# Kernel tuning notes

Hardware: AMD Instinct MI355X
Metric: run time of the kernel (lower is better)

The kernel has to match this reference:

```python
import jax, jax.numpy as jnp
import numpy as np

B, C, L, H, W, O = 1024, 256, 128, 256, 3, 256  # batch cols, channels, levels, hidden, window, output
N_LAYERS = 3


def setup_inputs() -> dict:
    key = jax.random.key(0)
    ks = jax.random.split(key, 12)
    in0 = C * W          # layer-0 input features after sliding window
    inr = 2 * H          # input features for layers > 0 (bi-dir concat)
    def wscale(fan_in):
        return 1.0 / np.sqrt(fan_in)
    inputs = jax.random.normal(ks[0], (B, C, L), dtype=jnp.float32)
    w_fw0 = jax.random.normal(ks[1], (in0 + H, 4 * H), jnp.float32) * wscale(in0 + H)
    b_fw0 = jnp.zeros((4 * H,), jnp.float32)
    w_bw0 = jax.random.normal(ks[2], (in0 + H, 4 * H), jnp.float32) * wscale(in0 + H)
    b_bw0 = jnp.zeros((4 * H,), jnp.float32)
    w_fw_rest = jax.random.normal(ks[3], (N_LAYERS - 1, inr + H, 4 * H), jnp.float32) * wscale(inr + H)
    b_fw_rest = jnp.zeros((N_LAYERS - 1, 4 * H), jnp.float32)
    w_bw_rest = jax.random.normal(ks[4], (N_LAYERS - 1, inr + H, 4 * H), jnp.float32) * wscale(inr + H)
    b_bw_rest = jnp.zeros((N_LAYERS - 1, 4 * H), jnp.float32)
    w_out = jax.random.normal(ks[5], (2 * H, O), jnp.float32) * wscale(2 * H)
    b_out = jnp.zeros((O,), jnp.float32)
    return dict(inputs=inputs, w_fw0=w_fw0, b_fw0=b_fw0, w_bw0=w_bw0, b_bw0=b_bw0,
                w_fw_rest=w_fw_rest, b_fw_rest=b_fw_rest, w_bw_rest=w_bw_rest,
                b_bw_rest=b_bw_rest, w_out=w_out, b_out=b_out)


def _lstm(xs, w, b, reverse):
    # xs: [L, B, F] time-major. haiku hk.LSTM gate order i, g, f, o with +1 forget bias.
    h0 = jnp.zeros((xs.shape[1], H), xs.dtype)
    def step(carry, x):
        h, c = carry
        gated = jnp.concatenate([x, h], axis=-1) @ w + b
        i, g, f, o = jnp.split(gated, 4, axis=-1)
        c = jax.nn.sigmoid(f + 1.0) * c + jax.nn.sigmoid(i) * jnp.tanh(g)
        h = jax.nn.sigmoid(o) * jnp.tanh(c)
        return (h, c), h
    _, ys = jax.lax.scan(step, (h0, h0), xs, reverse=reverse)
    return ys  # [L, B, H], aligned with input positions (matches hk.dynamic_unroll reverse)


def reference(inputs, w_fw0, b_fw0, w_bw0, b_bw0, w_fw_rest, b_fw_rest,
              w_bw_rest, b_bw_rest, w_out, b_out):
    x = jnp.swapaxes(inputs, 1, 2)  # [B, L, C] (original transposes [C, L] -> [L, C])
    # sliding_window_reshape over the level axis
    pad_start = (W - 1) // 2
    pad_end = W - 1 - pad_start
    xp = jnp.pad(x, ((0, 0), (pad_start, pad_end), (0, 0)))
    idx = jnp.arange(W)[None, :] + jnp.arange(L)[:, None]  # [L, W]
    xw = xp[:, idx, :]                                     # [B, L, W, C]
    xw = xw.reshape(x.shape[0], L, W * C)                  # row-major (window, channel) flatten
    xs = jnp.swapaxes(xw, 0, 1)                            # [L, B, W*C] time-major

    fw = _lstm(xs, w_fw0, b_fw0, reverse=False)
    bw = _lstm(xs, w_bw0, b_bw0, reverse=True)
    xs = jnp.concatenate([fw, bw], axis=-1)                # [L, B, 2H]
    for k in range(N_LAYERS - 1):
        fw = _lstm(xs, w_fw_rest[k], b_fw_rest[k], reverse=False)
        bw = _lstm(xs, w_bw_rest[k], b_bw_rest[k], reverse=True)
        xs = jnp.concatenate([fw, bw], axis=-1)

    out = xs @ w_out + b_out                               # [L, B, O]
    return jnp.transpose(out, (1, 2, 0))                   # [B, O, L] (original returns [O, L])
```

## Files before the change

kernel.cpp:

```cpp
#include <hip/hip_runtime.h>
#include <cstdint>

#define DEVI __device__ __forceinline__

typedef __bf16 bf16x8 __attribute__((ext_vector_type(8)));
typedef float f32x4 __attribute__((ext_vector_type(4)));

DEVI unsigned short f2b(float f) {
    unsigned int u = __builtin_bit_cast(unsigned int, f);
    unsigned int r = (u + 0x7FFFu + ((u >> 16) & 1u)) >> 16;
    return (unsigned short)r;
}
DEVI float b2f(unsigned short h) {
    unsigned int u = ((unsigned int)h) << 16;
    return __builtin_bit_cast(float, u);
}
DEVI float sigm(float x) { return 1.0f / (1.0f + __expf(-x)); }
DEVI float tanh_f(float x) {
    float e = __expf(-2.0f * fabsf(x));
    float r = (1.0f - e) / (1.0f + e);
    return x < 0.0f ? -r : r;
}

DEVI void gload_lds16(const unsigned short* g, unsigned short* l) {
    typedef __attribute__((address_space(1))) void gv_t;
    typedef __attribute__((address_space(3))) void lv_t;
    gv_t* gp = (gv_t*)(uintptr_t)g;
    lv_t* lp = (lv_t*)(unsigned int)(uintptr_t)l;
    __builtin_amdgcn_global_load_lds(gp, lp, 16, 0, 0);
}

__global__ void k_tin(const float* __restrict__ in, unsigned short* __restrict__ xT) {
    __shared__ float tile[32][33];
    int c0 = blockIdx.x * 32, t0 = blockIdx.y * 32, b = blockIdx.z;
    int tx = threadIdx.x, ty = threadIdx.y;
#pragma unroll
    for (int i = 0; i < 4; ++i) {
        int c = c0 + ty + i * 8;
        int t = t0 + tx;
        float v = 0.0f;
        if (t >= 1 && t <= 128) v = in[((size_t)b * 256 + c) * 128 + (t - 1)];
        tile[ty + i * 8][tx] = v;
    }
    __syncthreads();
#pragma unroll
    for (int i = 0; i < 4; ++i) {
        int t = t0 + ty + i * 8;
        int c = c0 + tx;
        if (t < 130) xT[((size_t)t * 1024 + b) * 256 + c] = f2b(tile[tx][ty + i * 8]);
    }
}

__global__ void k_wt(const float* __restrict__ w, unsigned short* __restrict__ wt, int K, int N) {
    __shared__ float tile[32][33];
    int n0 = blockIdx.x * 32, k0 = blockIdx.y * 32;
    int tx = threadIdx.x, ty = threadIdx.y;
#pragma unroll
    for (int i = 0; i < 4; ++i)
        tile[ty + i * 8][tx] = w[(size_t)(k0 + ty + i * 8) * N + n0 + tx];
    __syncthreads();
#pragma unroll
    for (int i = 0; i < 4; ++i)
        wt[(size_t)(n0 + ty + i * 8) * K + k0 + tx] = f2b(tile[tx][ty + i * 8]);
}

#define BM 128
#define BN 128
#define BKg 64

template <int MODE, int F32OUT, int BIAS>
__global__ __launch_bounds__(256) void kgemm(const unsigned short* __restrict__ A,
                                             const unsigned short* __restrict__ Wt,
                                             void* __restrict__ Cout,
                                             const float* __restrict__ bias,
                                             int Mtiles, int Ntiles, int KT, int strideA,
                                             int strideB, int N, int tbase) {
    __shared__ unsigned short As[BM * BKg];
    __shared__ unsigned short Bs[BN * BKg];

    int nwg = Mtiles * Ntiles;
    int q = nwg >> 3;
    int orig = blockIdx.x;
    int wg = (orig & 7) * q + (orig >> 3);
    int tn = wg % Ntiles, tm = wg / Ntiles;

    int tid = threadIdx.x;
    int wid = tid >> 6, lane = tid & 63;
    int srow = lane >> 3, skb = lane & 7;
    int lh = lane & 15, lq = lane >> 4;

    f32x4 acc[4][4] = {};
    int m0 = tm * BM;
    int t0 = m0 >> 10, b0 = m0 & 1023;
    int wr = wid >> 1, wc = wid & 1;

    for (int k0 = 0; k0 < KT; k0 += BKg) {
        const unsigned short* Abase;
        int rs;
        if (MODE == 1) {
            int w = k0 >> 8, c0 = k0 & 255;
            Abase = A + ((size_t)((tbase + t0 + w) * 1024 + b0)) * 256 + c0;
            rs = 256;
        } else {
            Abase = A + (size_t)m0 * strideA + k0;
            rs = strideA;
        }
        const unsigned short* Bbase = Wt + (size_t)(tn * BN) * strideB + k0;
#pragma unroll
        for (int c = 0; c < 4; ++c) {
            int chunk = c * 4 + wid;
            int row = chunk * 8 + srow;
            int kbs = skb ^ (row & 7);
            gload_lds16(Abase + (size_t)row * rs + kbs * 8, &As[chunk * 512]);
        }
#pragma unroll
        for (int c = 0; c < 4; ++c) {
            int chunk = c * 4 + wid;
            int row = chunk * 8 + srow;
            int kbs = skb ^ (row & 7);
            gload_lds16(Bbase + (size_t)row * strideB + kbs * 8, &Bs[chunk * 512]);
        }
        __syncthreads();
#pragma unroll
        for (int kk = 0; kk < 2; ++kk) {
            bf16x8 af[4], bfv[4];
            int kc = kk * 4 + lq;
#pragma unroll
            for (int i = 0; i < 4; ++i) {
                int m = wr * 64 + i * 16 + lh;
                af[i] = *(const bf16x8*)((const char*)As + m * 128 + ((kc ^ (m & 7)) * 16));
            }
#pragma unroll
            for (int j = 0; j < 4; ++j) {
                int n = wc * 64 + j * 16 + lh;
                bfv[j] = *(const bf16x8*)((const char*)Bs + n * 128 + ((kc ^ (n & 7)) * 16));
            }
#pragma unroll
            for (int i = 0; i < 4; ++i)
#pragma unroll
                for (int j = 0; j < 4; ++j)
                    acc[i][j] = __builtin_amdgcn_mfma_f32_16x16x32_bf16(af[i], bfv[j], acc[i][j], 0, 0, 0);
        }
        __syncthreads();
    }
#pragma unroll
    for (int i = 0; i < 4; ++i) {
#pragma unroll
        for (int j = 0; j < 4; ++j) {
            int colg = tn * BN + wc * 64 + j * 16 + lh;
            float bv = BIAS ? bias[colg] : 0.0f;
#pragma unroll
            for (int r = 0; r < 4; ++r) {
                int rowg = m0 + wr * 64 + i * 16 + lq * 4 + r;
                float v = acc[i][j][r] + bv;
                if (F32OUT)
                    ((float*)Cout)[(size_t)rowg * N + colg] = v;
                else
                    ((unsigned short*)Cout)[(size_t)rowg * N + colg] = f2b(v);
            }
        }
    }
}

__global__ __launch_bounds__(512) void klstm(const unsigned short* __restrict__ gxf,
                                             const unsigned short* __restrict__ gxb,
                                             const unsigned short* __restrict__ wtf,
                                             const unsigned short* __restrict__ wtb,
                                             const float* __restrict__ bf_,
                                             const float* __restrict__ bb_,
                                             unsigned short* __restrict__ xs_out,
                                             unsigned short* __restrict__ hst,
                                             float* __restrict__ cst,
                                             int I, int KS, int s0, int Tc) {
    __shared__ unsigned short h_lds[32 * 256];
    int dir = blockIdx.y;
    int b0 = blockIdx.x * 32;
    const unsigned short* gx = dir ? gxb : gxf;
    const unsigned short* wt = dir ? wtb : wtf;
    const float* bias = dir ? bb_ : bf_;
    const unsigned short* wh = wt + I;

    int tid = threadIdx.x, wid = tid >> 6, lane = tid & 63;
    int lh = lane & 15, lq = lane >> 4;

    float c_reg[2][2][4] = {};
    if (s0 == 0) {
        for (int i = tid; i < 32 * 256; i += 512) h_lds[i] = 0;
    } else {
        for (int i = tid; i < 32 * 256; i += 512) {
            int row = i >> 8, col = i & 255;
            *(unsigned short*)((char*)h_lds + row * 512 + (((col >> 3) ^ (row & 7)) * 16) +
                               (col & 7) * 2) = hst[((size_t)dir * 1024 + b0 + row) * 256 + col];
        }
#pragma unroll
        for (int mf = 0; mf < 2; ++mf)
#pragma unroll
            for (int r = 0; r < 4; ++r)
#pragma unroll
                for (int p = 0; p < 2; ++p) {
                    int row = mf * 16 + lq * 4 + r;
                    int col = wid * 32 + p * 16 + lh;
                    c_reg[mf][p][r] = cst[((size_t)dir * 1024 + b0 + row) * 256 + col];
                }
    }
    float bia[2], big[2], bif[2], bio[2];
#pragma unroll
    for (int p = 0; p < 2; ++p) {
        int col = wid * 32 + p * 16 + lh;
        bia[p] = bias[col];
        big[p] = bias[256 + col];
        bif[p] = bias[512 + col];
        bio[p] = bias[768 + col];
    }
    __syncthreads();

    for (int s = s0; s < s0 + Tc; ++s) {
        int t = dir ? (127 - s) : s;
        int gloc = dir ? (s0 + Tc - 1 - s) : (s - s0);

        bf16x8 afr[2][8];
#pragma unroll
        for (int mf = 0; mf < 2; ++mf)
#pragma unroll
            for (int kf = 0; kf < 8; ++kf) {
                int m = mf * 16 + lh;
                int kc = kf * 4 + lq;
                afr[mf][kf] = *(const bf16x8*)((const char*)h_lds + m * 512 + ((kc ^ (m & 7)) * 16));
            }
        __syncthreads();

        f32x4 acc[2][8] = {};
#pragma unroll
        for (int kf = 0; kf < 8; ++kf) {
#pragma unroll
            for (int nf = 0; nf < 8; ++nf) {
                int g = nf >> 1, p = nf & 1;
                int n = g * 256 + wid * 32 + p * 16 + lh;
                bf16x8 bfr = *(const bf16x8*)(wh + (size_t)n * KS + kf * 32 + lq * 8);
                acc[0][nf] = __builtin_amdgcn_mfma_f32_16x16x32_bf16(afr[0][kf], bfr, acc[0][nf], 0, 0, 0);
                acc[1][nf] = __builtin_amdgcn_mfma_f32_16x16x32_bf16(afr[1][kf], bfr, acc[1][nf], 0, 0, 0);
            }
        }

#pragma unroll
        for (int mf = 0; mf < 2; ++mf) {
#pragma unroll
            for (int r = 0; r < 4; ++r) {
                int row = mf * 16 + lq * 4 + r;
                size_t gxrow = ((size_t)gloc * 1024 + b0 + row) * 1024;
#pragma unroll
                for (int p = 0; p < 2; ++p) {
                    int col = wid * 32 + p * 16 + lh;
                    float gi = acc[mf][0 + p][r] + b2f(gx[gxrow + col]) + bia[p];
                    float gg = acc[mf][2 + p][r] + b2f(gx[gxrow + 256 + col]) + big[p];
                    float gf = acc[mf][4 + p][r] + b2f(gx[gxrow + 512 + col]) + bif[p];
                    float go = acc[mf][6 + p][r] + b2f(gx[gxrow + 768 + col]) + bio[p];
                    float cv = sigm(gf + 1.0f) * c_reg[mf][p][r] + sigm(gi) * tanh_f(gg);
                    c_reg[mf][p][r] = cv;
                    float hv = sigm(go) * tanh_f(cv);
                    unsigned short hb = f2b(hv);
                    *(unsigned short*)((char*)h_lds + row * 512 + (((col >> 3) ^ (row & 7)) * 16) +
                                       (col & 7) * 2) = hb;
                    xs_out[((size_t)t * 1024 + b0 + row) * 512 + dir * 256 + col] = hb;
                }
            }
        }
        __syncthreads();
    }

    for (int i = tid; i < 32 * 256; i += 512) {
        int row = i >> 8, col = i & 255;
        hst[((size_t)dir * 1024 + b0 + row) * 256 + col] =
            *(const unsigned short*)((const char*)h_lds + row * 512 +
                                     (((col >> 3) ^ (row & 7)) * 16) + (col & 7) * 2);
    }
#pragma unroll
    for (int mf = 0; mf < 2; ++mf)
#pragma unroll
        for (int r = 0; r < 4; ++r)
#pragma unroll
            for (int p = 0; p < 2; ++p) {
                int row = mf * 16 + lq * 4 + r;
                int col = wid * 32 + p * 16 + lh;
                cst[((size_t)dir * 1024 + b0 + row) * 256 + col] = c_reg[mf][p][r];
            }
}

__global__ void k_tout(const float* __restrict__ tmp, float* __restrict__ out) {
    __shared__ float tile[32][33];
    int o0 = blockIdx.x * 32, l0 = blockIdx.y * 32, b = blockIdx.z;
    int tx = threadIdx.x, ty = threadIdx.y;
#pragma unroll
    for (int i = 0; i < 4; ++i)
        tile[ty + i * 8][tx] = tmp[((size_t)(l0 + ty + i * 8) * 1024 + b) * 256 + o0 + tx];
    __syncthreads();
#pragma unroll
    for (int i = 0; i < 4; ++i)
        out[((size_t)b * 256 + o0 + ty + i * 8) * 128 + l0 + tx] = tile[tx][ty + i * 8];
}

extern "C" void kernel_launch(void* const* d_in, const int* in_sizes, int n_in,
                              void* d_out, int out_size, void* d_ws, size_t ws_size,
                              hipStream_t stream) {
    const float* inp  = (const float*)d_in[0];
    const float* wfw0 = (const float*)d_in[1];
    const float* bfw0 = (const float*)d_in[2];
    const float* wbw0 = (const float*)d_in[3];
    const float* bbw0 = (const float*)d_in[4];
    const float* wfwr = (const float*)d_in[5];
    const float* bfwr = (const float*)d_in[6];
    const float* wbwr = (const float*)d_in[7];
    const float* bbwr = (const float*)d_in[8];
    const float* wout = (const float*)d_in[9];
    const float* bout = (const float*)d_in[10];

    char* ws = (char*)d_ws;
    size_t o = 0;
    auto alloc = [&](size_t bytes) {
        void* p = ws + o;
        o += (bytes + 255) & ~(size_t)255;
        return p;
    };
    unsigned short* wt0f = (unsigned short*)alloc((size_t)1024 * 1024 * 2);
    unsigned short* wt0b = (unsigned short*)alloc((size_t)1024 * 1024 * 2);
    unsigned short* wt1f = (unsigned short*)alloc((size_t)1024 * 768 * 2);
    unsigned short* wt1b = (unsigned short*)alloc((size_t)1024 * 768 * 2);
    unsigned short* wt2f = (unsigned short*)alloc((size_t)1024 * 768 * 2);
    unsigned short* wt2b = (unsigned short*)alloc((size_t)1024 * 768 * 2);
    unsigned short* wto  = (unsigned short*)alloc((size_t)256 * 512 * 2);
    unsigned short* hst  = (unsigned short*)alloc((size_t)2 * 1024 * 256 * 2);
    float*          cst  = (float*)alloc((size_t)2 * 1024 * 256 * 4);
    unsigned short* xsa  = (unsigned short*)alloc((size_t)131072 * 512 * 2);
    unsigned short* xsb  = (unsigned short*)alloc((size_t)131072 * 512 * 2);
    unsigned short* xT   = xsb;
    float*          otmp = (float*)xsb;

    size_t base = o;
    int Tc = 128;
    while (Tc > 1 && base + (size_t)Tc * 4 * 1024 * 1024 > ws_size) Tc >>= 1;
    unsigned short* gxf = (unsigned short*)alloc((size_t)Tc * 1024 * 1024 * 2);
    unsigned short* gxb = (unsigned short*)alloc((size_t)Tc * 1024 * 1024 * 2);

    dim3 tb(32, 8);
    k_tin<<<dim3(8, 5, 1024), tb, 0, stream>>>(inp, xT);
    k_wt<<<dim3(32, 32), tb, 0, stream>>>(wfw0, wt0f, 1024, 1024);
    k_wt<<<dim3(32, 32), tb, 0, stream>>>(wbw0, wt0b, 1024, 1024);
    k_wt<<<dim3(32, 24), tb, 0, stream>>>(wfwr, wt1f, 768, 1024);
    k_wt<<<dim3(32, 24), tb, 0, stream>>>(wbwr, wt1b, 768, 1024);
    k_wt<<<dim3(32, 24), tb, 0, stream>>>(wfwr + (size_t)768 * 1024, wt2f, 768, 1024);
    k_wt<<<dim3(32, 24), tb, 0, stream>>>(wbwr + (size_t)768 * 1024, wt2b, 768, 1024);
    k_wt<<<dim3(8, 16), tb, 0, stream>>>(wout, wto, 512, 256);

    int Mt = Tc * 8, grid = Tc * 64;
    for (int s0 = 0; s0 < 128; s0 += Tc) {
        int tbw = 128 - s0 - Tc;
        kgemm<1, 0, 0><<<grid, 256, 0, stream>>>(xT, wt0f, gxf, nullptr, Mt, 8, 768, 256, 1024, 1024, s0);
        kgemm<1, 0, 0><<<grid, 256, 0, stream>>>(xT, wt0b, gxb, nullptr, Mt, 8, 768, 256, 1024, 1024, tbw);
        klstm<<<dim3(32, 2), 512, 0, stream>>>(gxf, gxb, wt0f, wt0b, bfw0, bbw0, xsa, hst, cst, 768, 1024, s0, Tc);
    }
    for (int s0 = 0; s0 < 128; s0 += Tc) {
        int tbw = 128 - s0 - Tc;
        kgemm<0, 0, 0><<<grid, 256, 0, stream>>>(xsa + (size_t)s0 * 1024 * 512, wt1f, gxf, nullptr, Mt, 8, 512, 512, 768, 1024, 0);
        kgemm<0, 0, 0><<<grid, 256, 0, stream>>>(xsa + (size_t)tbw * 1024 * 512, wt1b, gxb, nullptr, Mt, 8, 512, 512, 768, 1024, 0);
        klstm<<<dim3(32, 2), 512, 0, stream>>>(gxf, gxb, wt1f, wt1b, bfwr, bbwr, xsb, hst, cst, 512, 768, s0, Tc);
    }
    for (int s0 = 0; s0 < 128; s0 += Tc) {
        int tbw = 128 - s0 - Tc;
        kgemm<0, 0, 0><<<grid, 256, 0, stream>>>(xsb + (size_t)s0 * 1024 * 512, wt2f, gxf, nullptr, Mt, 8, 512, 512, 768, 1024, 0);
        kgemm<0, 0, 0><<<grid, 256, 0, stream>>>(xsb + (size_t)tbw * 1024 * 512, wt2b, gxb, nullptr, Mt, 8, 512, 512, 768, 1024, 0);
        klstm<<<dim3(32, 2), 512, 0, stream>>>(gxf, gxb, wt2f, wt2b, bfwr + 1024, bbwr + 1024, xsa, hst, cst, 512, 768, s0, Tc);
    }
    kgemm<0, 1, 1><<<2048, 256, 0, stream>>>(xsa, wto, otmp, bout, 1024, 2, 512, 512, 512, 256, 0);
    k_tout<<<dim3(8, 4, 1024), tb, 0, stream>>>(otmp, (float*)d_out);
}
```

Baseline: 9.077 ms.

## Fuse input projection into persistent bidirectional LSTM kernel with double-buffered x staging

Drops the separate per-chunk input-projection GEMMs, the gx buffers and the h/c state save/restore. A single 64-block kernel per layer now runs all 128 steps, multiplying the concatenated [x, h] by the full weight each step. The next timestep's input is prefetched into LDS with async global-to-LDS loads while the current step computes. This removes the gate-preactivation round trip through memory and many launches. In exchange, the non-recurrent GEMM work is serialized onto only 64 workgroups, and far more weight bytes are read from cache per step. Sigmoid and tanh divisions are also swapped for hardware reciprocal.

```diff
diff --git a/kernel.cpp b/kernel.cpp
--- a/kernel.cpp
+++ b/kernel.cpp
@@ -11,14 +11,11 @@
     unsigned int r = (u + 0x7FFFu + ((u >> 16) & 1u)) >> 16;
     return (unsigned short)r;
 }
-DEVI float b2f(unsigned short h) {
-    unsigned int u = ((unsigned int)h) << 16;
-    return __builtin_bit_cast(float, u);
-}
-DEVI float sigm(float x) { return 1.0f / (1.0f + __expf(-x)); }
+DEVI float frcp(float x) { return __builtin_amdgcn_rcpf(x); }
+DEVI float sigm(float x) { return frcp(1.0f + __expf(-x)); }
 DEVI float tanh_f(float x) {
     float e = __expf(-2.0f * fabsf(x));
-    float r = (1.0f - e) / (1.0f + e);
+    float r = (1.0f - e) * frcp(1.0f + e);
     return x < 0.0f ? -r : r;
 }
 
@@ -162,47 +159,55 @@
     }
 }
 
-__global__ __launch_bounds__(512) void klstm(const unsigned short* __restrict__ gxf,
-                                             const unsigned short* __restrict__ gxb,
-                                             const unsigned short* __restrict__ wtf,
-                                             const unsigned short* __restrict__ wtb,
-                                             const float* __restrict__ bf_,
-                                             const float* __restrict__ bb_,
-                                             unsigned short* __restrict__ xs_out,
-                                             unsigned short* __restrict__ hst,
-                                             float* __restrict__ cst,
-                                             int I, int KS, int s0, int Tc) {
+template <int KX, int WIN>
+DEVI void stage_x(const unsigned short* __restrict__ xin, int t, int b0,
+                  unsigned short* xbuf, int tid) {
+    constexpr int CH = KX / 16;
+    int wid = tid >> 6, lane = tid & 63;
+#pragma unroll
+    for (int c = wid; c < CH; c += 8) {
+        int e = c * 512 + lane * 8;
+        int row = e / KX;
+        int slot = (e - row * KX) >> 3;
+        int ss = (slot & ~7) | ((slot & 7) ^ (row & 7));
+        int col = ss << 3;
+        const unsigned short* src;
+        if (WIN) {
+            int w = col >> 8, cc = col & 255;
+            src = xin + ((size_t)((t + w) * 1024 + b0 + row)) * 256 + cc;
+        } else {
+            src = xin + ((size_t)t * 1024 + b0 + row) * (size_t)KX + col;
+        }
+        gload_lds16(src, xbuf + c * 512);
+    }
+}
+
+template <int KX, int WIN>
+__global__ __launch_bounds__(512) void klstm_f(const unsigned short* __restrict__ xin,
+                                               const unsigned short* __restrict__ wtf,
+                                               const unsigned short* __restrict__ wtb,
+                                               const float* __restrict__ bf_,
+                                               const float* __restrict__ bb_,
+                                               unsigned short* __restrict__ xs_out) {
+    constexpr int KS = KX + 256;
+    constexpr int KF_X = KX / 32;
     __shared__ unsigned short h_lds[32 * 256];
-    int dir = blockIdx.y;
-    int b0 = blockIdx.x * 32;
-    const unsigned short* gx = dir ? gxb : gxf;
+    __shared__ unsigned short xb[2][32 * KX];
+
+    int bid = blockIdx.x;
+    int xcd = bid & 7;
+    int dir = xcd >> 2;
+    int idx = (bid >> 3) * 4 + (xcd & 3);
+    int b0 = idx * 32;
     const unsigned short* wt = dir ? wtb : wtf;
     const float* bias = dir ? bb_ : bf_;
-    const unsigned short* wh = wt + I;
 
     int tid = threadIdx.x, wid = tid >> 6, lane = tid & 63;
     int lh = lane & 15, lq = lane >> 4;
 
+    for (int i = tid; i < 32 * 256; i += 512) h_lds[i] = 0;
+
     float c_reg[2][2][4] = {};
-    if (s0 == 0) {
-        for (int i = tid; i < 32 * 256; i += 512) h_lds[i] = 0;
-    } else {
-        for (int i = tid; i < 32 * 256; i += 512) {
-            int row = i >> 8, col = i & 255;
-            *(unsigned short*)((char*)h_lds + row * 512 + (((col >> 3) ^ (row & 7)) * 16) +
-                               (col & 7) * 2) = hst[((size_t)dir * 1024 + b0 + row) * 256 + col];
-        }
-#pragma unroll
-        for (int mf = 0; mf < 2; ++mf)
-#pragma unroll
-            for (int r = 0; r < 4; ++r)
-#pragma unroll
-                for (int p = 0; p < 2; ++p) {
-                    int row = mf * 16 + lq * 4 + r;
-                    int col = wid * 32 + p * 16 + lh;
-                    c_reg[mf][p][r] = cst[((size_t)dir * 1024 + b0 + row) * 256 + col];
-                }
-    }
     float bia[2], big[2], bif[2], bio[2];
 #pragma unroll
     for (int p = 0; p < 2; ++p) {
@@ -212,49 +217,75 @@
         bif[p] = bias[512 + col];
         bio[p] = bias[768 + col];
     }
+    stage_x<KX, WIN>(xin, dir ? 127 : 0, b0, &xb[0][0], tid);
     __syncthreads();
 
-    for (int s = s0; s < s0 + Tc; ++s) {
+    for (int s = 0; s < 128; ++s) {
         int t = dir ? (127 - s) : s;
-        int gloc = dir ? (s0 + Tc - 1 - s) : (s - s0);
-
-        bf16x8 afr[2][8];
-#pragma unroll
-        for (int mf = 0; mf < 2; ++mf)
-#pragma unroll
-            for (int kf = 0; kf < 8; ++kf) {
-                int m = mf * 16 + lh;
-                int kc = kf * 4 + lq;
-                afr[mf][kf] = *(const bf16x8*)((const char*)h_lds + m * 512 + ((kc ^ (m & 7)) * 16));
-            }
-        __syncthreads();
+        int tnx = dir ? (t > 0 ? t - 1 : 0) : (t < 127 ? t + 1 : 127);
+        const unsigned short* xcur = &xb[s & 1][0];
+
+        stage_x<KX, WIN>(xin, tnx, b0, &xb[(s & 1) ^ 1][0], tid);
 
         f32x4 acc[2][8] = {};
-#pragma unroll
-        for (int kf = 0; kf < 8; ++kf) {
+#pragma unroll 4
+        for (int kf = 0; kf < KF_X; ++kf) {
+            int kc = kf * 4 + lq;
+            bf16x8 a0, a1;
+            {
+                int m = lh;
+                int ss = (kc & ~7) | ((kc & 7) ^ (m & 7));
+                a0 = *(const bf16x8*)((const char*)xcur + m * (KX * 2) + ss * 16);
+            }
+            {
+                int m = 16 + lh;
+                int ss = (kc & ~7) | ((kc & 7) ^ (m & 7));
+                a1 = *(const bf16x8*)((const char*)xcur + m * (KX * 2) + ss * 16);
+            }
 #pragma unroll
             for (int nf = 0; nf < 8; ++nf) {
                 int g = nf >> 1, p = nf & 1;
                 int n = g * 256 + wid * 32 + p * 16 + lh;
-                bf16x8 bfr = *(const bf16x8*)(wh + (size_t)n * KS + kf * 32 + lq * 8);
-                acc[0][nf] = __builtin_amdgcn_mfma_f32_16x16x32_bf16(afr[0][kf], bfr, acc[0][nf], 0, 0, 0);
-                acc[1][nf] = __builtin_amdgcn_mfma_f32_16x16x32_bf16(afr[1][kf], bfr, acc[1][nf], 0, 0, 0);
-            }
-        }
+                bf16x8 bfr = *(const bf16x8*)(wt + (size_t)n * KS + kf * 32 + lq * 8);
+                acc[0][nf] = __builtin_amdgcn_mfma_f32_16x16x32_bf16(a0, bfr, acc[0][nf], 0, 0, 0);
+                acc[1][nf] = __builtin_amdgcn_mfma_f32_16x16x32_bf16(a1, bfr, acc[1][nf], 0, 0, 0);
+            }
+        }
+#pragma unroll
+        for (int kf = 0; kf < 8; ++kf) {
+            int kc = kf * 4 + lq;
+            bf16x8 a0, a1;
+            {
+                int m = lh;
+                a0 = *(const bf16x8*)((const char*)h_lds + m * 512 + ((kc ^ (m & 7)) * 16));
+            }
+            {
+                int m = 16 + lh;
+                a1 = *(const bf16x8*)((const char*)h_lds + m * 512 + ((kc ^ (m & 7)) * 16));
+            }
+#pragma unroll
+            for (int nf = 0; nf < 8; ++nf) {
+                int g = nf >> 1, p = nf & 1;
+                int n = g * 256 + wid * 32 + p * 16 + lh;
+                bf16x8 bfr = *(const bf16x8*)(wt + (size_t)n * KS + KX + kf * 32 + lq * 8);
+                acc[0][nf] = __builtin_amdgcn_mfma_f32_16x16x32_bf16(a0, bfr, acc[0][nf], 0, 0, 0);
+                acc[1][nf] = __builtin_amdgcn_mfma_f32_16x16x32_bf16(a1, bfr, acc[1][nf], 0, 0, 0);
+            }
+        }
+        __syncthreads();
 
 #pragma unroll
         for (int mf = 0; mf < 2; ++mf) {
 #pragma unroll
             for (int r = 0; r < 4; ++r) {
                 int row = mf * 16 + lq * 4 + r;
-                size_t gxrow = ((size_t)gloc * 1024 + b0 + row) * 1024;
 #pragma unroll
                 for (int p = 0; p < 2; ++p) {
                     int col = wid * 32 + p * 16 + lh;
-                    float gi = acc[mf][0 + p][r] + b2f(gx[gxrow + col]) + bia[p];
-                    float gg = acc[mf][2 + p][r] + b2f(gx[gxrow + 256 + col]) + big[p];
-                    float gf = acc[mf][4 + p][r] + b2f(gx[gxrow + 512 + col]) + bif[p];
-                    float go = acc[mf][6 + p][r] + b2f(gx[gxrow + 768 + col]) + bio[p];
+                    float gi = acc[mf][0 + p][r] + bia[p];
+                    float gg = acc[mf][2 + p][r] + big[p];
+                    float gf = acc[mf][4 + p][r] + bif[p];
+                    float go = acc[mf][6 + p][r] + bio[p];
                     float cv = sigm(gf + 1.0f) * c_reg[mf][p][r] + sigm(gi) * tanh_f(gg);
                     c_reg[mf][p][r] = cv;
                     float hv = sigm(go) * tanh_f(cv);
@@ -267,23 +298,6 @@
         }
         __syncthreads();
     }
-
-    for (int i = tid; i < 32 * 256; i += 512) {
-        int row = i >> 8, col = i & 255;
-        hst[((size_t)dir * 1024 + b0 + row) * 256 + col] =
-            *(const unsigned short*)((const char*)h_lds + row * 512 +
-                                     (((col >> 3) ^ (row & 7)) * 16) + (col & 7) * 2);
-    }
-#pragma unroll
-    for (int mf = 0; mf < 2; ++mf)
-#pragma unroll
-        for (int r = 0; r < 4; ++r)
-#pragma unroll
-            for (int p = 0; p < 2; ++p) {
-                int row = mf * 16 + lq * 4 + r;
-                int col = wid * 32 + p * 16 + lh;
-                cst[((size_t)dir * 1024 + b0 + row) * 256 + col] = c_reg[mf][p][r];
-            }
 }
 
 __global__ void k_tout(const float* __restrict__ tmp, float* __restrict__ out) {
@@ -328,18 +342,10 @@
     unsigned short* wt2f = (unsigned short*)alloc((size_t)1024 * 768 * 2);
     unsigned short* wt2b = (unsigned short*)alloc((size_t)1024 * 768 * 2);
     unsigned short* wto  = (unsigned short*)alloc((size_t)256 * 512 * 2);
-    unsigned short* hst  = (unsigned short*)alloc((size_t)2 * 1024 * 256 * 2);
-    float*          cst  = (float*)alloc((size_t)2 * 1024 * 256 * 4);
     unsigned short* xsa  = (unsigned short*)alloc((size_t)131072 * 512 * 2);
-    unsigned short* xsb  = (unsigned short*)alloc((size_t)131072 * 512 * 2);
-    unsigned short* xT   = xsb;
-    float*          otmp = (float*)xsb;
-
-    size_t base = o;
-    int Tc = 128;
-    while (Tc > 1 && base + (size_t)Tc * 4 * 1024 * 1024 > ws_size) Tc >>= 1;
-    unsigned short* gxf = (unsigned short*)alloc((size_t)Tc * 1024 * 1024 * 2);
-    unsigned short* gxb = (unsigned short*)alloc((size_t)Tc * 1024 * 1024 * 2);
+    unsigned short* xsbR = (unsigned short*)alloc((size_t)131072 * 512 * 2);
+    unsigned short* xT   = xsbR;
+    float*          otmp = (float*)xsbR;
 
     dim3 tb(32, 8);
     k_tin<<<dim3(8, 5, 1024), tb, 0, stream>>>(inp, xT);
@@ -351,25 +357,10 @@
     k_wt<<<dim3(32, 24), tb, 0, stream>>>(wbwr + (size_t)768 * 1024, wt2b, 768, 1024);
     k_wt<<<dim3(8, 16), tb, 0, stream>>>(wout, wto, 512, 256);
 
-    int Mt = Tc * 8, grid = Tc * 64;
-    for (int s0 = 0; s0 < 128; s0 += Tc) {
-        int tbw = 128 - s0 - Tc;
-        kgemm<1, 0, 0><<<grid, 256, 0, stream>>>(xT, wt0f, gxf, nullptr, Mt, 8, 768, 256, 1024, 1024, s0);
-        kgemm<1, 0, 0><<<grid, 256, 0, stream>>>(xT, wt0b, gxb, nullptr, Mt, 8, 768, 256, 1024, 1024, tbw);
-        klstm<<<dim3(32, 2), 512, 0, stream>>>(gxf, gxb, wt0f, wt0b, bfw0, bbw0, xsa, hst, cst, 768, 1024, s0, Tc);
-    }
-    for (int s0 = 0; s0 < 128; s0 += Tc) {
-        int tbw = 128 - s0 - Tc;
-        kgemm<0, 0, 0><<<grid, 256, 0, stream>>>(xsa + (size_t)s0 * 1024 * 512, wt1f, gxf, nullptr, Mt, 8, 512, 512, 768, 1024, 0);
-        kgemm<0, 0, 0><<<grid, 256, 0, stream>>>(xsa + (size_t)tbw * 1024 * 512, wt1b, gxb, nullptr, Mt, 8, 512, 512, 768, 1024, 0);
-        klstm<<<dim3(32, 2), 512, 0, stream>>>(gxf, gxb, wt1f, wt1b, bfwr, bbwr, xsb, hst, cst, 512, 768, s0, Tc);
-    }
-    for (int s0 = 0; s0 < 128; s0 += Tc) {
-        int tbw = 128 - s0 - Tc;
-        kgemm<0, 0, 0><<<grid, 256, 0, stream>>>(xsb + (size_t)s0 * 1024 * 512, wt2f, gxf, nullptr, Mt, 8, 512, 512, 768, 1024, 0);
-        kgemm<0, 0, 0><<<grid, 256, 0, stream>>>(xsb + (size_t)tbw * 1024 * 512, wt2b, gxb, nullptr, Mt, 8, 512, 512, 768, 1024, 0);
-        klstm<<<dim3(32, 2), 512, 0, stream>>>(gxf, gxb, wt2f, wt2b, bfwr + 1024, bbwr + 1024, xsa, hst, cst, 512, 768, s0, Tc);
-    }
+    klstm_f<768, 1><<<64, 512, 0, stream>>>(xT, wt0f, wt0b, bfw0, bbw0, xsa);
+    klstm_f<512, 0><<<64, 512, 0, stream>>>(xsa, wt1f, wt1b, bfwr, bbwr, xsbR);
+    klstm_f<512, 0><<<64, 512, 0, stream>>>(xsbR, wt2f, wt2b, bfwr + 1024, bbwr + 1024, xsa);
+
     kgemm<0, 1, 1><<<2048, 256, 0, stream>>>(xsa, wto, otmp, bout, 1024, 2, 512, 512, 512, 256, 0);
     k_tout<<<dim3(8, 4, 1024), tb, 0, stream>>>(otmp, (float*)d_out);
 }
```

After: 22.69 ms. +149.9%, slower.

## Split LSTM weights, fuse fw/bw input GEMMs, software-pipeline recurrent MFMA loads

Applied to the files above, without the earlier changes.

Splits each layer's weights into separate input and recurrent blocks, with forward and backward stacked. When the workspace allows, one GEMM per layer computes both directions' input projections into an interleaved 2048-wide buffer. The recurrent kernel now streams recurrent weights through a three-slot register ring and H fragments through a double buffer, overlapping global and LDS loads with MFMAs, and it prefetches the gate inputs before the activations. Sigmoid and tanh use a hardware reciprocal instead of division, which adds register pressure and slightly lowers accuracy.

```diff
diff --git a/kernel.cpp b/kernel.cpp
--- a/kernel.cpp
+++ b/kernel.cpp
@@ -15,10 +15,11 @@
     unsigned int u = ((unsigned int)h) << 16;
     return __builtin_bit_cast(float, u);
 }
-DEVI float sigm(float x) { return 1.0f / (1.0f + __expf(-x)); }
+DEVI float frcp(float x) { return __builtin_amdgcn_rcpf(x); }
+DEVI float sigm(float x) { return frcp(1.0f + __expf(-x)); }
 DEVI float tanh_f(float x) {
     float e = __expf(-2.0f * fabsf(x));
-    float r = (1.0f - e) / (1.0f + e);
+    float r = (1.0f - e) * frcp(1.0f + e);
     return x < 0.0f ? -r : r;
 }
 
@@ -162,23 +163,20 @@
     }
 }
 
-__global__ __launch_bounds__(512) void klstm(const unsigned short* __restrict__ gxf,
-                                             const unsigned short* __restrict__ gxb,
-                                             const unsigned short* __restrict__ wtf,
-                                             const unsigned short* __restrict__ wtb,
-                                             const float* __restrict__ bf_,
-                                             const float* __restrict__ bb_,
-                                             unsigned short* __restrict__ xs_out,
-                                             unsigned short* __restrict__ hst,
-                                             float* __restrict__ cst,
-                                             int I, int KS, int s0, int Tc) {
+__global__ __launch_bounds__(512, 2) void klstm_p(const unsigned short* __restrict__ gxf,
+                                                  const unsigned short* __restrict__ gxb, int GS,
+                                                  const unsigned short* __restrict__ wth,
+                                                  const float* __restrict__ bf_,
+                                                  const float* __restrict__ bb_,
+                                                  unsigned short* __restrict__ xs_out,
+                                                  unsigned short* __restrict__ hst,
+                                                  float* __restrict__ cst, int s0, int Tc) {
     __shared__ unsigned short h_lds[32 * 256];
     int dir = blockIdx.y;
     int b0 = blockIdx.x * 32;
     const unsigned short* gx = dir ? gxb : gxf;
-    const unsigned short* wt = dir ? wtb : wtf;
+    const unsigned short* wh = wth + (size_t)dir * 1024 * 256;
     const float* bias = dir ? bb_ : bf_;
-    const unsigned short* wh = wt + I;
 
     int tid = threadIdx.x, wid = tid >> 6, lane = tid & 63;
     int lh = lane & 15, lq = lane >> 4;
@@ -212,49 +210,82 @@
         bif[p] = bias[512 + col];
         bio[p] = bias[768 + col];
     }
+    const unsigned short* wb[8];
+#pragma unroll
+    for (int nf = 0; nf < 8; ++nf) {
+        int g = nf >> 1, p = nf & 1;
+        int n = g * 256 + wid * 32 + p * 16 + lh;
+        wb[nf] = wh + (size_t)n * 256 + lq * 8;
+    }
     __syncthreads();
 
     for (int s = s0; s < s0 + Tc; ++s) {
         int t = dir ? (127 - s) : s;
         int gloc = dir ? (s0 + Tc - 1 - s) : (s - s0);
 
-        bf16x8 afr[2][8];
+        f32x4 acc[2][8] = {};
+        bf16x8 wreg[3][8];
+        bf16x8 afr[2][2];
+
+#define LDW(KF, SLOT)                                                       \
+    {                                                                       \
+        _Pragma("unroll") for (int nf = 0; nf < 8; ++nf) wreg[SLOT][nf] =   \
+            *(const bf16x8*)(wb[nf] + (KF)*32);                             \
+    }
+#define LDA(KF, SLOT)                                                        \
+    {                                                                        \
+        int kc = (KF)*4 + lq;                                                \
+        _Pragma("unroll") for (int mf = 0; mf < 2; ++mf) {                   \
+            int m = mf * 16 + lh;                                            \
+            afr[SLOT][mf] = *(const bf16x8*)((const char*)h_lds + m * 512 +  \
+                                             ((kc ^ (m & 7)) * 16));         \
+        }                                                                    \
+    }
+        LDW(0, 0);
+        LDW(1, 1);
+        LDA(0, 0);
+#pragma unroll
+        for (int kf = 0; kf < 8; ++kf) {
+            if (kf < 6) LDW(kf + 2, (kf + 2) % 3);
+            if (kf < 7) LDA(kf + 1, (kf + 1) & 1);
+#pragma unroll
+            for (int nf = 0; nf < 8; ++nf) {
+                acc[0][nf] = __builtin_amdgcn_mfma_f32_16x16x32_bf16(afr[kf & 1][0], wreg[kf % 3][nf],
+                                                                    acc[0][nf], 0, 0, 0);
+                acc[1][nf] = __builtin_amdgcn_mfma_f32_16x16x32_bf16(afr[kf & 1][1], wreg[kf % 3][nf],
+                                                                    acc[1][nf], 0, 0, 0);
+            }
+        }
+#undef LDW
+#undef LDA
+        __syncthreads();
+
+        unsigned short gu[2][2][4][4];
 #pragma unroll
         for (int mf = 0; mf < 2; ++mf)
-#pragma unroll
-            for (int kf = 0; kf < 8; ++kf) {
-                int m = mf * 16 + lh;
-                int kc = kf * 4 + lq;
-                afr[mf][kf] = *(const bf16x8*)((const char*)h_lds + m * 512 + ((kc ^ (m & 7)) * 16));
-            }
-        __syncthreads();
-
-        f32x4 acc[2][8] = {};
-#pragma unroll
-        for (int kf = 0; kf < 8; ++kf) {
-#pragma unroll
-            for (int nf = 0; nf < 8; ++nf) {
-                int g = nf >> 1, p = nf & 1;
-                int n = g * 256 + wid * 32 + p * 16 + lh;
-                bf16x8 bfr = *(const bf16x8*)(wh + (size_t)n * KS + kf * 32 + lq * 8);
-                acc[0][nf] = __builtin_amdgcn_mfma_f32_16x16x32_bf16(afr[0][kf], bfr, acc[0][nf], 0, 0, 0);
-                acc[1][nf] = __builtin_amdgcn_mfma_f32_16x16x32_bf16(afr[1][kf], bfr, acc[1][nf], 0, 0, 0);
-            }
-        }
-
-#pragma unroll
-        for (int mf = 0; mf < 2; ++mf) {
 #pragma unroll
             for (int r = 0; r < 4; ++r) {
                 int row = mf * 16 + lq * 4 + r;
-                size_t gxrow = ((size_t)gloc * 1024 + b0 + row) * 1024;
+                const unsigned short* gp = gx + ((size_t)gloc * 1024 + b0 + row) * GS;
 #pragma unroll
                 for (int p = 0; p < 2; ++p) {
                     int col = wid * 32 + p * 16 + lh;
-                    float gi = acc[mf][0 + p][r] + b2f(gx[gxrow + col]) + bia[p];
-                    float gg = acc[mf][2 + p][r] + b2f(gx[gxrow + 256 + col]) + big[p];
-                    float gf = acc[mf][4 + p][r] + b2f(gx[gxrow + 512 + col]) + bif[p];
-                    float go = acc[mf][6 + p][r] + b2f(gx[gxrow + 768 + col]) + bio[p];
+#pragma unroll
+                    for (int g = 0; g < 4; ++g) gu[mf][p][r][g] = gp[g * 256 + col];
+                }
+            }
+#pragma unroll
+        for (int mf = 0; mf < 2; ++mf) {
+#pragma unroll
+            for (int r = 0; r < 4; ++r) {
+                int row = mf * 16 + lq * 4 + r;
+#pragma unroll
+                for (int p = 0; p < 2; ++p) {
+                    int col = wid * 32 + p * 16 + lh;
+                    float gi = acc[mf][0 + p][r] + b2f(gu[mf][p][r][0]) + bia[p];
+                    float gg = acc[mf][2 + p][r] + b2f(gu[mf][p][r][1]) + big[p];
+                    float gf = acc[mf][4 + p][r] + b2f(gu[mf][p][r][2]) + bif[p];
+                    float go = acc[mf][6 + p][r] + b2f(gu[mf][p][r][3]) + bio[p];
                     float cv = sigm(gf + 1.0f) * c_reg[mf][p][r] + sigm(gi) * tanh_f(gg);
                     c_reg[mf][p][r] = cv;
                     float hv = sigm(go) * tanh_f(cv);
@@ -321,55 +352,73 @@
         o += (bytes + 255) & ~(size_t)255;
         return p;
     };
-    unsigned short* wt0f = (unsigned short*)alloc((size_t)1024 * 1024 * 2);
-    unsigned short* wt0b = (unsigned short*)alloc((size_t)1024 * 1024 * 2);
-    unsigned short* wt1f = (unsigned short*)alloc((size_t)1024 * 768 * 2);
-    unsigned short* wt1b = (unsigned short*)alloc((size_t)1024 * 768 * 2);
-    unsigned short* wt2f = (unsigned short*)alloc((size_t)1024 * 768 * 2);
-    unsigned short* wt2b = (unsigned short*)alloc((size_t)1024 * 768 * 2);
+    unsigned short* wtx0 = (unsigned short*)alloc((size_t)2048 * 768 * 2);
+    unsigned short* wtx1 = (unsigned short*)alloc((size_t)2048 * 512 * 2);
+    unsigned short* wtx2 = (unsigned short*)alloc((size_t)2048 * 512 * 2);
+    unsigned short* wth0 = (unsigned short*)alloc((size_t)2048 * 256 * 2);
+    unsigned short* wth1 = (unsigned short*)alloc((size_t)2048 * 256 * 2);
+    unsigned short* wth2 = (unsigned short*)alloc((size_t)2048 * 256 * 2);
     unsigned short* wto  = (unsigned short*)alloc((size_t)256 * 512 * 2);
     unsigned short* hst  = (unsigned short*)alloc((size_t)2 * 1024 * 256 * 2);
     float*          cst  = (float*)alloc((size_t)2 * 1024 * 256 * 4);
     unsigned short* xsa  = (unsigned short*)alloc((size_t)131072 * 512 * 2);
-    unsigned short* xsb  = (unsigned short*)alloc((size_t)131072 * 512 * 2);
-    unsigned short* xT   = xsb;
-    float*          otmp = (float*)xsb;
+    unsigned short* xsbR = (unsigned short*)alloc((size_t)131072 * 512 * 2);
+    unsigned short* xT   = xsbR;
+    float*          otmp = (float*)xsbR;
 
     size_t base = o;
     int Tc = 128;
-    while (Tc > 1 && base + (size_t)Tc * 4 * 1024 * 1024 > ws_size) Tc >>= 1;
-    unsigned short* gxf = (unsigned short*)alloc((size_t)Tc * 1024 * 1024 * 2);
-    unsigned short* gxb = (unsigned short*)alloc((size_t)Tc * 1024 * 1024 * 2);
+    while (Tc > 1 && base + (size_t)Tc * 1024 * 2048 * 2 > ws_size) Tc >>= 1;
+    bool fused = (Tc == 128);
+    unsigned short* gx  = (unsigned short*)alloc((size_t)Tc * 1024 * 2048 * 2);
+    unsigned short* gxB = gx + (size_t)Tc * 1024 * 1024;
 
     dim3 tb(32, 8);
     k_tin<<<dim3(8, 5, 1024), tb, 0, stream>>>(inp, xT);
-    k_wt<<<dim3(32, 32), tb, 0, stream>>>(wfw0, wt0f, 1024, 1024);
-    k_wt<<<dim3(32, 32), tb, 0, stream>>>(wbw0, wt0b, 1024, 1024);
-    k_wt<<<dim3(32, 24), tb, 0, stream>>>(wfwr, wt1f, 768, 1024);
-    k_wt<<<dim3(32, 24), tb, 0, stream>>>(wbwr, wt1b, 768, 1024);
-    k_wt<<<dim3(32, 24), tb, 0, stream>>>(wfwr + (size_t)768 * 1024, wt2f, 768, 1024);
-    k_wt<<<dim3(32, 24), tb, 0, stream>>>(wbwr + (size_t)768 * 1024, wt2b, 768, 1024);
+    k_wt<<<dim3(32, 24), tb, 0, stream>>>(wfw0, wtx0, 768, 1024);
+    k_wt<<<dim3(32, 24), tb, 0, stream>>>(wbw0, wtx0 + (size_t)1024 * 768, 768, 1024);
+    k_wt<<<dim3(32, 8), tb, 0, stream>>>(wfw0 + (size_t)768 * 1024, wth0, 256, 1024);
+    k_wt<<<dim3(32, 8), tb, 0, stream>>>(wbw0 + (size_t)768 * 1024, wth0 + (size_t)1024 * 256, 256, 1024);
+    for (int k = 0; k < 2; ++k) {
+        unsigned short* wtx = k ? wtx2 : wtx1;
+        unsigned short* wth_ = k ? wth2 : wth1;
+        const float* wf = wfwr + (size_t)k * 768 * 1024;
+        const float* wbk = wbwr + (size_t)k * 768 * 1024;
+        k_wt<<<dim3(32, 16), tb, 0, stream>>>(wf, wtx, 512, 1024);
+        k_wt<<<dim3(32, 16), tb, 0, stream>>>(wbk, wtx + (size_t)1024 * 512, 512, 1024);
+        k_wt<<<dim3(32, 8), tb, 0, stream>>>(wf + (size_t)512 * 1024, wth_, 256, 1024);
+        k_wt<<<dim3(32, 8), tb, 0, stream>>>(wbk + (size_t)512 * 1024, wth_ + (size_t)1024 * 256, 256, 1024);
+    }
     k_wt<<<dim3(8, 16), tb, 0, stream>>>(wout, wto, 512, 256);
 
-    int Mt = Tc * 8, grid = Tc * 64;
-    for (int s0 = 0; s0 < 128; s0 += Tc) {
-        int tbw = 128 - s0 - Tc;
-        kgemm<1, 0, 0><<<grid, 256, 0, stream>>>(xT, wt0f, gxf, nullptr, Mt, 8, 768, 256, 1024, 1024, s0);
-        kgemm<1, 0, 0><<<grid, 256, 0, stream>>>(xT, wt0b, gxb, nullptr, Mt, 8, 768, 256, 1024, 1024, tbw);
-        klstm<<<dim3(32, 2), 512, 0, stream>>>(gxf, gxb, wt0f, wt0b, bfw0, bbw0, xsa, hst, cst, 768, 1024, s0, Tc);
-    }
-    for (int s0 = 0; s0 < 128; s0 += Tc) {
-        int tbw = 128 - s0 - Tc;
-        kgemm<0, 0, 0><<<grid, 256, 0, stream>>>(xsa + (size_t)s0 * 1024 * 512, wt1f, gxf, nullptr, Mt, 8, 512, 512, 768, 1024, 0);
-        kgemm<0, 0, 0><<<grid, 256, 0, stream>>>(xsa + (size_t)tbw * 1024 * 512, wt1b, gxb, nullptr, Mt, 8, 512, 512, 768, 1024, 0);
-        klstm<<<dim3(32, 2), 512, 0, stream>>>(gxf, gxb, wt1f, wt1b, bfwr, bbwr, xsb, hst, cst, 512, 768, s0, Tc);
-    }
-    for (int s0 = 0; s0 < 128; s0 += Tc) {
-        int tbw = 128 - s0 - Tc;
-        kgemm<0, 0, 0><<<grid, 256, 0, stream>>>(xsb + (size_t)s0 * 1024 * 512, wt2f, gxf, nullptr, Mt, 8, 512, 512, 768, 1024, 0);
-        kgemm<0, 0, 0><<<grid, 256, 0, stream>>>(xsb + (size_t)tbw * 1024 * 512, wt2b, gxb, nullptr, Mt, 8, 512, 512, 768, 1024, 0);
-        klstm<<<dim3(32, 2), 512, 0, stream>>>(gxf, gxb, wt2f, wt2b, bfwr + 1024, bbwr + 1024, xsa, hst, cst, 512, 768, s0, Tc);
-    }
+    auto layer = [&](const unsigned short* xin, int KX, bool win, unsigned short* wtx,
+                     unsigned short* wth_, const float* bfp, const float* bbp,
+                     unsigned short* xout) {
+        if (fused) {
+            if (win)
+                kgemm<1, 0, 0><<<16384, 256, 0, stream>>>(xin, wtx, gx, nullptr, 1024, 16, KX, 256, KX, 2048, 0);
+            else
+                kgemm<0, 0, 0><<<16384, 256, 0, stream>>>(xin, wtx, gx, nullptr, 1024, 16, KX, KX, KX, 2048, 0);
+            klstm_p<<<dim3(32, 2), 512, 0, stream>>>(gx, gx + 1024, 2048, wth_, bfp, bbp, xout, hst, cst, 0, 128);
+        } else {
+            for (int s0 = 0; s0 < 128; s0 += Tc) {
+                int tbw = 128 - s0 - Tc;
+                if (win) {
+                    kgemm<1, 0, 0><<<Tc * 64, 256, 0, stream>>>(xin, wtx, gx, nullptr, Tc * 8, 8, KX, 256, KX, 1024, s0);
+                    kgemm<1, 0, 0><<<Tc * 64, 256, 0, stream>>>(xin, wtx + (size_t)1024 * KX, gxB, nullptr, Tc * 8, 8, KX, 256, KX, 1024, tbw);
+                } else {
+                    kgemm<0, 0, 0><<<Tc * 64, 256, 0, stream>>>(xin + (size_t)s0 * 1024 * KX, wtx, gx, nullptr, Tc * 8, 8, KX, KX, KX, 1024, 0);
+                    kgemm<0, 0, 0><<<Tc * 64, 256, 0, stream>>>(xin + (size_t)tbw * 1024 * KX, wtx + (size_t)1024 * KX, gxB, nullptr, Tc * 8, 8, KX, KX, KX, 1024, 0);
+                }
+                klstm_p<<<dim3(32, 2), 512, 0, stream>>>(gx, gxB, 1024, wth_, bfp, bbp, xout, hst, cst, s0, Tc);
+            }
+        }
+    };
+
+    layer(xT, 768, true, wtx0, wth0, bfw0, bbw0, xsa);
+    layer(xsa, 512, false, wtx1, wth1, bfwr, bbwr, xsbR);
+    layer(xsbR, 512, false, wtx2, wth2, bfwr + 1024, bbwr + 1024, xsa);
+
     kgemm<0, 1, 1><<<2048, 256, 0, stream>>>(xsa, wto, otmp, bout, 1024, 2, 512, 512, 512, 256, 0);
     k_tout<<<dim3(8, 4, 1024), tb, 0, stream>>>(otmp, (float*)d_out);
 }
```

After: 8.663 ms. 1.05x faster.
